# Kernel tuning notes

Measured on AMD Instinct MI355X. Metric: run time of the kernel, lower is better.

Reference implementation:

```python
import jax, jax.numpy as jnp
import numpy as np

FEAT_STRIDE = 8
BASE_SCALES = jnp.array([16.0, 9.0, 14.0, 21.0, 33.0, 54.0, 93.0], dtype=jnp.float32)
SCALE = 1.0
N_PRE_NMS = 6000
N_POST_NMS = 300
NMS_THRESH = 0.7
MIN_SIZE = 16.0


def setup_inputs() -> dict:
    key = jax.random.key(0)
    ks = jax.random.split(key, 8)
    C, M, H, W = 512, 512, 128, 128
    return {
        "x": jax.random.normal(ks[0], (1, C, H, W), jnp.float32),
        "skeleton_mask": jax.random.randint(ks[1], (H, W), 0, 2).astype(jnp.int32),
        "conv1_w": jax.random.normal(ks[2], (M, C, 3, 3), jnp.float32) * 0.01,
        "conv1_b": jnp.zeros((M,), jnp.float32),
        "loc_w": jax.random.normal(ks[3], (4, M), jnp.float32) * 0.01,
        "loc_b": jnp.zeros((4,), jnp.float32),
        "cls_w": jax.random.normal(ks[4], (7, M), jnp.float32) * 0.01,
        "cls_b": jnp.zeros((7,), jnp.float32),
        "cos_w": jax.random.normal(ks[5], (1, M), jnp.float32) * 0.01,
        "cos_b": jnp.zeros((1,), jnp.float32),
        "img_h": 1024,
        "img_w": 1024,
    }


def _loc2bbox(anchor, loc):
    # anchor, loc: (R,4) yxyx / (dy,dx,dh,dw)
    h = anchor[:, 2] - anchor[:, 0]
    w = anchor[:, 3] - anchor[:, 1]
    cy = anchor[:, 0] + 0.5 * h
    cx = anchor[:, 1] + 0.5 * w
    ncy = loc[:, 0] * h + cy
    ncx = loc[:, 1] * w + cx
    nh = jnp.exp(loc[:, 2]) * h
    nw = jnp.exp(loc[:, 3]) * w
    return jnp.stack([ncy - 0.5 * nh, ncx - 0.5 * nw, ncy + 0.5 * nh, ncx + 0.5 * nw], axis=1)


def _nms(boxes, scores, thresh, n_out):
    # greedy NMS with fixed number of output slots (jit-compatible)
    ys0, xs0, ys1, xs1 = boxes[:, 0], boxes[:, 1], boxes[:, 2], boxes[:, 3]
    areas = (ys1 - ys0) * (xs1 - xs0)

    def body(k, state):
        live, keep_idx, keep_valid = state
        s = jnp.where(live, scores, -jnp.inf)
        i = jnp.argmax(s)
        valid = s[i] > -jnp.inf
        yy0 = jnp.maximum(ys0, boxes[i, 0])
        xx0 = jnp.maximum(xs0, boxes[i, 1])
        yy1 = jnp.minimum(ys1, boxes[i, 2])
        xx1 = jnp.minimum(xs1, boxes[i, 3])
        inter = jnp.maximum(yy1 - yy0, 0.0) * jnp.maximum(xx1 - xx0, 0.0)
        iou = inter / (areas + areas[i] - inter + 1e-9)
        live = live & (iou <= thresh)  # removes i itself (iou==1)
        keep_idx = keep_idx.at[k].set(jnp.where(valid, i, 0).astype(jnp.int32))
        keep_valid = keep_valid.at[k].set(valid)
        return live, keep_idx, keep_valid

    live0 = jnp.ones(boxes.shape[0], dtype=bool)
    idx0 = jnp.zeros((n_out,), jnp.int32)
    val0 = jnp.zeros((n_out,), bool)
    _, keep_idx, keep_valid = jax.lax.fori_loop(0, n_out, body, (live0, idx0, val0))
    return keep_idx, keep_valid


def reference(x, skeleton_mask, conv1_w, conv1_b, loc_w, loc_b, cls_w, cls_b, cos_w, cos_b, img_h, img_w):
    n, C, hh, ww = x.shape
    # conv1 + relu + skeleton attention mask (broadcast over all channels as in repeat)
    h = jax.lax.conv_general_dilated(
        x, conv1_w, window_strides=(1, 1), padding="SAME",
        dimension_numbers=("NCHW", "OIHW", "NCHW")) + conv1_b[None, :, None, None]
    h = jax.nn.relu(h) * skeleton_mask.astype(h.dtype)[None, None, :, :]

    # 1x1 heads as einsum
    rpn_locs = (jnp.einsum("nchw,oc->nhwo", h, loc_w) + loc_b).reshape(n, -1, 4)
    rpn_cos = jax.nn.sigmoid(jnp.einsum("nchw,oc->nhwo", h, cos_w) + cos_b).reshape(n, -1, 1)
    rpn_cls = jnp.einsum("nchw,oc->nhwo", h, cls_w) + cls_b  # (n, hh, ww, 7)
    p = jax.nn.softmax(rpn_cls, axis=-1)
    rpn_fg_scores = (1.0 - p[..., 0]).reshape(n, -1)
    rpn_cls_flat = rpn_cls.reshape(-1, 7)
    p_flat = p.reshape(-1, 7)

    # anchor generation (data dependent)
    assignment = jnp.argmax(p_flat, axis=1)                    # (HW,)
    ascale = BASE_SCALES[assignment] * SCALE
    acos = rpn_cos[0, :, 0]
    acos = jnp.where(acos == 0, acos + 1e-5, acos)
    hvec = ascale * jnp.sqrt(1.0 / (acos * acos) - 1.0)
    anchor_h = jnp.full_like(ascale, hvec[0])  # faithful to original _cos2hw [0] broadcast
    anchor_w = ascale
    sy, sx = jnp.meshgrid(jnp.arange(hh, dtype=jnp.float32) * FEAT_STRIDE,
                          jnp.arange(ww, dtype=jnp.float32) * FEAT_STRIDE, indexing="ij")
    ay = sy.ravel() + FEAT_STRIDE / 2.0
    ax = sx.ravel() + FEAT_STRIDE / 2.0
    anchor = jnp.stack([ay - 0.5 * anchor_h, ax - 0.5 * anchor_w,
                        ay + 0.5 * anchor_h, ax + 0.5 * anchor_w], axis=1)

    # keepa: only anchors assigned to a foreground scale class (mask instead of gather)
    keep_mask = assignment > 0

    # ProposalCreator: decode, clip, min-size filter, top-k, NMS
    roi = _loc2bbox(anchor, rpn_locs[0])
    roi = jnp.stack([jnp.clip(roi[:, 0], 0.0, float(img_h)),
                     jnp.clip(roi[:, 1], 0.0, float(img_w)),
                     jnp.clip(roi[:, 2], 0.0, float(img_h)),
                     jnp.clip(roi[:, 3], 0.0, float(img_w))], axis=1)
    hs = roi[:, 2] - roi[:, 0]
    ws = roi[:, 3] - roi[:, 1]
    valid = keep_mask & (hs >= MIN_SIZE * SCALE) & (ws >= MIN_SIZE * SCALE)
    scores = jnp.where(valid, rpn_fg_scores[0], -jnp.inf)

    top_scores, order = jax.lax.top_k(scores, N_PRE_NMS)
    cand = roi[order]                                           # (N_PRE_NMS, 4)
    cand = jnp.where(jnp.isfinite(top_scores)[:, None], cand, 0.0)
    keep_idx, keep_valid = _nms(cand, top_scores, NMS_THRESH, N_POST_NMS)

    rois = jnp.where(keep_valid[:, None], cand[keep_idx], 0.0)   # (N_POST_NMS, 4) padded
    roi_scores = jnp.where(keep_valid, top_scores[keep_idx], 0.0)
    roi_indices = jnp.zeros((N_POST_NMS,), jnp.int32)
    old_rois = cand                                              # pre-NMS candidates

    return (rpn_locs, rois, roi_indices, anchor, rpn_cls_flat, rpn_cos, roi_scores, old_rois)
```

## Files before the change

kernel.cpp:

```cpp
#include <hip/hip_runtime.h>
#include <math.h>

#define HH 128
#define WW 128
#define CIN 512
#define NPIX 16384
#define NPRE 6000
#define NPOST 300
#define NMW 94

#define WS_XS1    0ull
#define WS_XS2    4194304ull
#define WS_XS3    8388608ull
#define WS_WB1    12582912ull
#define WS_WB2    13762560ull
#define WS_WB3    14942208ull
#define WS_LIST   16121856ull
#define WS_NACT   16138240ull
#define WS_MASK   16138248ull
#define WS_LOG    17266248ull
#define WS_ROI    17659464ull
#define WS_SC32   17725000ull
#define WS_CAND   17741384ull
#define WS_TOPS   17765384ull

#define O_LOCS   0
#define O_ROIS   65536
#define O_RIDX   66736
#define O_ANCHOR 67036
#define O_CLS    132572
#define O_COS    247260
#define O_RSC    263644
#define O_OLD    263944

typedef short bf16x8 __attribute__((ext_vector_type(8)));
typedef float f32x4 __attribute__((ext_vector_type(4)));

__device__ __forceinline__ float exp32(float x) { return (float)exp((double)x); }
__device__ __forceinline__ float sqrt32(float x) { return (float)sqrt((double)x); }

__device__ __forceinline__ unsigned short bf16t(float v) {
  return (unsigned short)(__float_as_uint(v) >> 16);
}
__device__ __forceinline__ float bf2f(unsigned short u) {
  return __uint_as_float((unsigned)u << 16);
}
__device__ __forceinline__ void split3(float v, unsigned short& s1,
                                       unsigned short& s2, unsigned short& s3) {
  s1 = bf16t(v);
  float r = v - bf2f(s1);
  s2 = bf16t(r);
  float r2 = r - bf2f(s2);
  s3 = bf16t(r2);
}

__global__ __launch_bounds__(256) void prep_kernel(
    const float* __restrict__ x, const float* __restrict__ w,
    unsigned short* __restrict__ xs1, unsigned short* __restrict__ xs2,
    unsigned short* __restrict__ xs3, unsigned short* __restrict__ wb1,
    unsigned short* __restrict__ wb2, unsigned short* __restrict__ wb3,
    double* __restrict__ logits, const int* __restrict__ mask,
    int* __restrict__ list, int* __restrict__ nact) {
  int b = blockIdx.x;
  int tid = threadIdx.x;
  if (b < 2048) {
    __shared__ float t[64][65];
    int p0 = (b & 255) * 64;
    int c0 = (b >> 8) * 64;
    int lo = tid & 63;
    int q = tid >> 6;
#pragma unroll
    for (int ii = 0; ii < 16; ++ii) {
      int cc = q + ii * 4;
      t[cc][lo] = x[(size_t)(c0 + cc) * NPIX + p0 + lo];
    }
    __syncthreads();
#pragma unroll
    for (int ii = 0; ii < 16; ++ii) {
      int pp = q + ii * 4;
      float v = t[lo][pp];
      unsigned short s1, s2, s3;
      split3(v, s1, s2, s3);
      size_t addr = (size_t)(p0 + pp) * 512 + c0 + lo;
      xs1[addr] = s1; xs2[addr] = s2; xs3[addr] = s3;
    }
  } else if (b < 2495) {
    int i = (b - 2048) * 256 + tid;
    const int stride = 447 * 256;
    for (; i < NPIX * 12; i += stride) logits[i] = 0.0;
  } else if (b == 2495) {
    __shared__ int sc[256];
    int base = tid << 6;
    int cnt = 0;
    for (int i = 0; i < 64; ++i) cnt += (mask[base + i] != 0);
    sc[tid] = cnt;
    __syncthreads();
    for (int off = 1; off < 256; off <<= 1) {
      int v = 0;
      if (tid >= off) v = sc[tid - off];
      __syncthreads();
      sc[tid] += v;
      __syncthreads();
    }
    int pos = sc[tid] - cnt;
    for (int i = 0; i < 64; ++i)
      if (mask[base + i] != 0) list[pos++] = base + i;
    if (tid == 255) nact[0] = sc[255];
  } else {
    int id = (b - 2496) * 256 + tid;
    const int stride = 2048 * 256;
    for (; id < 9 * 512 * 512; id += stride) {
      int ce = id & 7;
      int oc = (id >> 3) & 511;
      int rest = id >> 12;
      int j = rest >> 6;
      int cb = rest & 63;
      int c = cb * 8 + ce;
      float v = w[(size_t)oc * 4608 + c * 9 + j];
      unsigned short s1, s2, s3;
      split3(v, s1, s2, s3);
      wb1[id] = s1; wb2[id] = s2; wb3[id] = s3;
    }
  }
}

__global__ __launch_bounds__(256, 2) void conv_bf16_kernel(
    const unsigned short* __restrict__ xs1, const unsigned short* __restrict__ xs2,
    const unsigned short* __restrict__ xs3, const unsigned short* __restrict__ wb1,
    const unsigned short* __restrict__ wb2, const unsigned short* __restrict__ wb3,
    const float* __restrict__ bias, const float* __restrict__ loc_w,
    const float* __restrict__ cls_w, const float* __restrict__ cos_w,
    const int* __restrict__ list, const int* __restrict__ nact,
    double* __restrict__ logits) {
  int tid = threadIdx.x;
  int lane = tid & 63;
  int wv = tid >> 6;
  int n = nact[0];
  int ntg = (n + 63) >> 6;
  int total = ntg << 3;
  int lin = blockIdx.x;
  int xcd = lin & 7;
  int slot = lin >> 3;
  int wpx = (total + 7) >> 3;
  int w = xcd * wpx + slot;
  if (slot >= wpx || w >= total) return;
  int tg = w >> 3;
  int m0 = (w & 7) << 6;
  int tile = tg * 4 + wv;
  if (tile * 16 >= n) return;
  int col = lane & 15;
  int kk = lane >> 4;

  int slotp = tile * 16 + col;
  int p = (slotp < n) ? list[slotp] : -1;
  bool pv = (p >= 0);
  int py = p >> 7, px = p & 127;

  int offj[9];
  bool valj[9];
#pragma unroll
  for (int j = 0; j < 9; ++j) {
    int dy = j / 3 - 1, dx = j % 3 - 1;
    int yy = py + dy, xx = px + dx;
    bool v = pv && (yy >= 0) && (yy < HH) && (xx >= 0) && (xx < WW);
    valj[j] = v;
    offj[j] = v ? (yy * WW + xx) : 0;
  }

  f32x4 acc[4];
#pragma unroll
  for (int nf = 0; nf < 4; ++nf) acc[nf] = (f32x4){0.f, 0.f, 0.f, 0.f};

  const bf16x8 zzv = (bf16x8){0, 0, 0, 0, 0, 0, 0, 0};
  int ka = kk * 8;
  int bcol[4];
#pragma unroll
  for (int nf = 0; nf < 4; ++nf) bcol[nf] = (m0 + nf * 16 + col) * 8;

  for (int c0 = 0; c0 < CIN; c0 += 32) {
    int kc = c0 + ka;
    int cb = kc >> 3;
#pragma unroll
    for (int j = 0; j < 9; ++j) {
      size_t axi = (size_t)offj[j] * 512 + kc;
      bf16x8 a1 = *(const bf16x8*)(xs1 + axi);
      bf16x8 a2 = *(const bf16x8*)(xs2 + axi);
      bf16x8 a3 = *(const bf16x8*)(xs3 + axi);
      a1 = valj[j] ? a1 : zzv;
      a2 = valj[j] ? a2 : zzv;
      a3 = valj[j] ? a3 : zzv;
      int wjb = (j * 64 + cb) * 4096;
      bf16x8 B1[4], B2[4], B3[4];
#pragma unroll
      for (int nf = 0; nf < 4; ++nf) {
        B1[nf] = *(const bf16x8*)(wb1 + wjb + bcol[nf]);
        B2[nf] = *(const bf16x8*)(wb2 + wjb + bcol[nf]);
        B3[nf] = *(const bf16x8*)(wb3 + wjb + bcol[nf]);
      }
#pragma unroll
      for (int nf = 0; nf < 4; ++nf)
        acc[nf] = __builtin_amdgcn_mfma_f32_16x16x32_bf16(a1, B1[nf], acc[nf], 0, 0, 0);
#pragma unroll
      for (int nf = 0; nf < 4; ++nf)
        acc[nf] = __builtin_amdgcn_mfma_f32_16x16x32_bf16(a1, B2[nf], acc[nf], 0, 0, 0);
#pragma unroll
      for (int nf = 0; nf < 4; ++nf)
        acc[nf] = __builtin_amdgcn_mfma_f32_16x16x32_bf16(a2, B1[nf], acc[nf], 0, 0, 0);
#pragma unroll
      for (int nf = 0; nf < 4; ++nf)
        acc[nf] = __builtin_amdgcn_mfma_f32_16x16x32_bf16(a1, B3[nf], acc[nf], 0, 0, 0);
#pragma unroll
      for (int nf = 0; nf < 4; ++nf)
        acc[nf] = __builtin_amdgcn_mfma_f32_16x16x32_bf16(a2, B2[nf], acc[nf], 0, 0, 0);
#pragma unroll
      for (int nf = 0; nf < 4; ++nf)
        acc[nf] = __builtin_amdgcn_mfma_f32_16x16x32_bf16(a3, B1[nf], acc[nf], 0, 0, 0);
    }
  }

#pragma unroll
  for (int jj = 0; jj < 4; ++jj) {
    float hvj[4];
#pragma unroll
    for (int nf = 0; nf < 4; ++nf) {
      float bb = bias[m0 + nf * 16 + col];
      hvj[nf] = fmaxf(__fadd_rn(acc[nf][jj], bb), 0.f);
    }
    int s2 = tile * 16 + kk * 4 + jj;
    bool wr = (col == 0) && (s2 < n);
    int pix = wr ? list[s2] : 0;
#pragma unroll
    for (int r = 0; r < 12; ++r) {
      double t = 0.0;
#pragma unroll
      for (int nf = 0; nf < 4; ++nf) {
        int oc = m0 + nf * 16 + col;
        float wh = (r < 4) ? loc_w[r * 512 + oc]
                           : (r < 11) ? cls_w[(r - 4) * 512 + oc] : cos_w[oc];
        t += (double)hvj[nf] * (double)wh;
      }
#pragma unroll
      for (int o = 8; o; o >>= 1) t += __shfl_xor(t, o, 16);
      if (wr) atomicAdd(&logits[(size_t)pix * 12 + r], t);
    }
  }
}

__global__ __launch_bounds__(256) void finroi_kernel(
    const double* __restrict__ logits, const float* __restrict__ loc_b,
    const float* __restrict__ cls_b, const float* __restrict__ cos_b,
    const int* __restrict__ img_h, const int* __restrict__ img_w,
    float* __restrict__ out, float* __restrict__ roi,
    float* __restrict__ scores32) {
  int p = blockIdx.x * 256 + threadIdx.x;
  const double* lg = &logits[(size_t)p * 12];
  float l4[4];
#pragma unroll
  for (int o = 0; o < 4; ++o) {
    l4[o] = (float)(lg[o] + (double)loc_b[o]);
    out[O_LOCS + p * 4 + o] = l4[o];
  }
  double cl[7];
#pragma unroll
  for (int i = 0; i < 7; ++i) {
    cl[i] = lg[4 + i] + (double)cls_b[i];
    out[O_CLS + p * 7 + i] = (float)cl[i];
  }
  double z = lg[11] + (double)cos_b[0];
  double sig = 1.0 / (1.0 + exp(-z));
  out[O_COS + p] = (float)sig;
  double pm = cl[0];
  int ai = 0;
#pragma unroll
  for (int i = 1; i < 7; ++i)
    if (cl[i] > pm) { pm = cl[i]; ai = i; }
  double mx = cl[0];
#pragma unroll
  for (int i = 1; i < 7; ++i) mx = fmax(mx, cl[i]);
  double S = 0.0;
#pragma unroll
  for (int i = 0; i < 7; ++i) S += exp(cl[i] - mx);
  double p0 = exp(cl[0] - mx) / S;
  float fg = (float)(1.0 - p0);
  const float BS[7] = {16.f, 9.f, 14.f, 21.f, 33.f, 54.f, 93.f};
  float ascale_p = BS[ai];
  double cl0[7];
#pragma unroll
  for (int i = 0; i < 7; ++i) cl0[i] = logits[4 + i] + (double)cls_b[i];
  double pm0 = cl0[0];
  int ai0 = 0;
#pragma unroll
  for (int i = 1; i < 7; ++i)
    if (cl0[i] > pm0) { pm0 = cl0[i]; ai0 = i; }
  float ascale0 = BS[ai0];
  double z0 = logits[11] + (double)cos_b[0];
  float a0 = (float)(1.0 / (1.0 + exp(-z0)));
  if (a0 == 0.0f) a0 = __fadd_rn(a0, 1e-5f);
  float t1 = __fmul_rn(a0, a0);
  float t2 = __fdiv_rn(1.0f, t1);
  float t3 = __fsub_rn(t2, 1.0f);
  float anchor_h = __fmul_rn(ascale0, sqrt32(t3));
  float anchor_w = ascale_p;
  float ay = __fadd_rn((float)(p >> 7) * 8.0f, 4.0f);
  float ax = __fadd_rn((float)(p & 127) * 8.0f, 4.0f);
  float A0 = __fsub_rn(ay, __fmul_rn(0.5f, anchor_h));
  float A1 = __fsub_rn(ax, __fmul_rn(0.5f, anchor_w));
  float A2 = __fadd_rn(ay, __fmul_rn(0.5f, anchor_h));
  float A3 = __fadd_rn(ax, __fmul_rn(0.5f, anchor_w));
  *(float4*)&out[O_ANCHOR + p * 4] = make_float4(A0, A1, A2, A3);
  float hA = __fsub_rn(A2, A0), wA = __fsub_rn(A3, A1);
  float cy = __fadd_rn(A0, __fmul_rn(0.5f, hA));
  float cx = __fadd_rn(A1, __fmul_rn(0.5f, wA));
  float ncy = __fadd_rn(__fmul_rn(l4[0], hA), cy);
  float ncx = __fadd_rn(__fmul_rn(l4[1], wA), cx);
  float nh = __fmul_rn(exp32(l4[2]), hA);
  float nw = __fmul_rn(exp32(l4[3]), wA);
  float b0 = __fsub_rn(ncy, __fmul_rn(0.5f, nh));
  float b1 = __fsub_rn(ncx, __fmul_rn(0.5f, nw));
  float b2 = __fadd_rn(ncy, __fmul_rn(0.5f, nh));
  float b3 = __fadd_rn(ncx, __fmul_rn(0.5f, nw));
  float IH = (float)img_h[0], IW = (float)img_w[0];
  b0 = fminf(fmaxf(b0, 0.f), IH);
  b1 = fminf(fmaxf(b1, 0.f), IW);
  b2 = fminf(fmaxf(b2, 0.f), IH);
  b3 = fminf(fmaxf(b3, 0.f), IW);
  *(float4*)&roi[p * 4] = make_float4(b0, b1, b2, b3);
  float hs = __fsub_rn(b2, b0), wd = __fsub_rn(b3, b1);
  bool valid = (ai > 0) && (hs >= 16.f) && (wd >= 16.f);
  scores32[p] = valid ? fg : -INFINITY;
}

__global__ __launch_bounds__(256) void rank_kernel(
    const float* __restrict__ scores32, const float* __restrict__ roi,
    float* __restrict__ out, float* __restrict__ cand, float* __restrict__ tops) {
  __shared__ unsigned long long kt[2048];
  int tid = threadIdx.x;
  int i = blockIdx.x * 256 + tid;
  unsigned u = __float_as_uint(scores32[i]);
  u = (u & 0x80000000u) ? ~u : (u | 0x80000000u);
  unsigned long long mykey = ((unsigned long long)u << 32) | (unsigned)(16383 - i);
  int rank = 0;
  for (int t0 = 0; t0 < 16384; t0 += 2048) {
    __syncthreads();
#pragma unroll
    for (int s = 0; s < 8; ++s) {
      int j = t0 + s * 256 + tid;
      unsigned uj = __float_as_uint(scores32[j]);
      uj = (uj & 0x80000000u) ? ~uj : (uj | 0x80000000u);
      kt[s * 256 + tid] = ((unsigned long long)uj << 32) | (unsigned)(16383 - j);
    }
    __syncthreads();
    for (int t = 0; t < 2048; ++t)
      rank += (kt[t] > mykey) ? 1 : 0;
  }
  if (rank < NPRE) {
    float s = scores32[i];
    float4 b = make_float4(0.f, 0.f, 0.f, 0.f);
    if (isfinite(s)) b = *(const float4*)&roi[i * 4];
    ((float4*)(out + O_OLD))[rank] = b;
    ((float4*)cand)[rank] = b;
    tops[rank] = s;
  }
}

__global__ __launch_bounds__(64) void nms_mask_kernel(
    const float* __restrict__ cand, unsigned long long* __restrict__ mask) {
  __shared__ float cy0[64], cx0[64], cy1[64], cx1[64], car[64];
  int bw = blockIdx.x;
  int bj = blockIdx.y;
  int t = threadIdx.x;
  int c = bw * 64 + t;
  if (c < NPRE) {
    float4 b = ((const float4*)cand)[c];
    cy0[t] = b.x; cx0[t] = b.y; cy1[t] = b.z; cx1[t] = b.w;
    car[t] = __fmul_rn(__fsub_rn(b.z, b.x), __fsub_rn(b.w, b.y));
  } else {
    cy0[t] = 0.f; cx0[t] = 0.f; cy1[t] = 0.f; cx1[t] = 0.f; car[t] = 0.f;
  }
  __syncthreads();
  int r = bj * 64 + t;
  if (r >= NPRE) return;
  float4 rb = ((const float4*)cand)[r];
  float rar = __fmul_rn(__fsub_rn(rb.z, rb.x), __fsub_rn(rb.w, rb.y));
  unsigned long long bits = 0;
#pragma unroll 4
  for (int b = 0; b < 64; ++b) {
    int j = bw * 64 + b;
    float yy0 = fmaxf(cy0[b], rb.x), xx0 = fmaxf(cx0[b], rb.y);
    float yy1 = fminf(cy1[b], rb.z), xx1 = fminf(cx1[b], rb.w);
    float inter = __fmul_rn(fmaxf(__fsub_rn(yy1, yy0), 0.f),
                            fmaxf(__fsub_rn(xx1, xx0), 0.f));
    float den = __fadd_rn(__fsub_rn(__fadd_rn(car[b], rar), inter), 1e-9f);
    float iou = __fdiv_rn(inter, den);
    if (j > r && j < NPRE && iou > 0.7f)
      bits |= 1ull << b;
  }
  mask[(size_t)r * NMW + bw] = bits;
}

__global__ __launch_bounds__(128) void nms_reduce_kernel(
    const float* __restrict__ cand, const float* __restrict__ tops,
    const unsigned long long* __restrict__ mask, float* __restrict__ out) {
  __shared__ unsigned long long remv[NMW];
  __shared__ int red2[2];
  int tid = threadIdx.x;
  int lane = tid & 63, wid = tid >> 6;
  if (tid < NMW) remv[tid] = 0ull;
  __syncthreads();
  int kdone = NPOST;
  for (int k = 0; k < NPOST; ++k) {
    int cnd = 0x7FFFFFFF;
    if (tid < NMW) {
      unsigned long long avail = ~remv[tid];
      if (tid == NMW - 1) avail &= (1ull << (NPRE - (NMW - 1) * 64)) - 1;
      if (avail) cnd = (tid << 6) + (int)__builtin_ctzll(avail);
    }
#pragma unroll
    for (int off = 32; off; off >>= 1) {
      int o = __shfl_xor(cnd, off, 64);
      cnd = min(cnd, o);
    }
    if (lane == 0) red2[wid] = cnd;
    __syncthreads();
    int pick = min(red2[0], red2[1]);
    bool valid = (pick != 0x7FFFFFFF) && (tops[pick] != -INFINITY);
    if (!valid) { kdone = k; break; }
    if (tid == 0) {
      float4 b = ((const float4*)cand)[pick];
      out[O_ROIS + k * 4 + 0] = b.x;
      out[O_ROIS + k * 4 + 1] = b.y;
      out[O_ROIS + k * 4 + 2] = b.z;
      out[O_ROIS + k * 4 + 3] = b.w;
      out[O_RSC + k] = tops[pick];
    }
    if (tid < NMW) {
      unsigned long long m = mask[(size_t)pick * NMW + tid];
      if (tid == (pick >> 6)) m |= 1ull << (pick & 63);
      remv[tid] |= m;
    }
    __syncthreads();
  }
  for (int t = kdone + tid; t < NPOST; t += 128) {
    out[O_ROIS + t * 4 + 0] = 0.f;
    out[O_ROIS + t * 4 + 1] = 0.f;
    out[O_ROIS + t * 4 + 2] = 0.f;
    out[O_ROIS + t * 4 + 3] = 0.f;
    out[O_RSC + t] = 0.f;
  }
  for (int t = tid; t < NPOST; t += 128) out[O_RIDX + t] = 0.f;
}

extern "C" void kernel_launch(void* const* d_in, const int* in_sizes, int n_in,
                              void* d_out, int out_size, void* d_ws, size_t ws_size,
                              hipStream_t stream) {
  (void)in_sizes; (void)n_in; (void)out_size; (void)ws_size;
  const float* x      = (const float*)d_in[0];
  const int*   skel   = (const int*)d_in[1];
  const float* conv_w = (const float*)d_in[2];
  const float* conv_b = (const float*)d_in[3];
  const float* loc_w  = (const float*)d_in[4];
  const float* loc_b  = (const float*)d_in[5];
  const float* cls_w  = (const float*)d_in[6];
  const float* cls_b  = (const float*)d_in[7];
  const float* cos_w  = (const float*)d_in[8];
  const float* cos_b  = (const float*)d_in[9];
  const int*   img_h  = (const int*)d_in[10];
  const int*   img_w  = (const int*)d_in[11];
  float* out = (float*)d_out;
  float* ws  = (float*)d_ws;

  unsigned short* xs1 = (unsigned short*)(ws + WS_XS1);
  unsigned short* xs2 = (unsigned short*)(ws + WS_XS2);
  unsigned short* xs3 = (unsigned short*)(ws + WS_XS3);
  unsigned short* wb1 = (unsigned short*)(ws + WS_WB1);
  unsigned short* wb2 = (unsigned short*)(ws + WS_WB2);
  unsigned short* wb3 = (unsigned short*)(ws + WS_WB3);
  int*    list     = (int*)(ws + WS_LIST);
  int*    nact     = (int*)(ws + WS_NACT);
  unsigned long long* nmsmask = (unsigned long long*)(ws + WS_MASK);
  double* logits   = (double*)(ws + WS_LOG);
  float*  roi      = ws + WS_ROI;
  float*  scores32 = ws + WS_SC32;
  float*  cand     = ws + WS_CAND;
  float*  tops     = ws + WS_TOPS;

  hipLaunchKernelGGL(prep_kernel, dim3(4544), dim3(256), 0, stream, x, conv_w,
                     xs1, xs2, xs3, wb1, wb2, wb3, logits, skel, list, nact);
  hipLaunchKernelGGL(conv_bf16_kernel, dim3(2048), dim3(256), 0, stream, xs1, xs2,
                     xs3, wb1, wb2, wb3, conv_b, loc_w, cls_w, cos_w, list, nact,
                     logits);
  hipLaunchKernelGGL(finroi_kernel, dim3(64), dim3(256), 0, stream, logits, loc_b,
                     cls_b, cos_b, img_h, img_w, out, roi, scores32);
  hipLaunchKernelGGL(rank_kernel, dim3(64), dim3(256), 0, stream, scores32, roi, out,
                     cand, tops);
  hipLaunchKernelGGL(nms_mask_kernel, dim3(NMW, NMW), dim3(64), 0, stream, cand,
                     nmsmask);
  hipLaunchKernelGGL(nms_reduce_kernel, dim3(1), dim3(128), 0, stream, cand, tops,
                     nmsmask, out);
}
```

Baseline: 1.070 ms.

## Process two 16-pixel tiles per wave to reuse weight fragments

Each wave now computes two 16-pixel subtiles against the same 64 output channels, so each loaded B fragment (three bf16 splits) feeds twice as many MFMAs and per-MFMA weight traffic is halved. Out-of-bounds neighbours now point at a zeroed padding row in the split-input buffers instead of using per-load selects, and the workspace offsets shift to make room for that row. The grid is halved to match. The cost is doubled accumulator and A-fragment registers, which may pressure occupancy under launch_bounds(256,2).

```diff
diff --git a/kernel.cpp b/kernel.cpp
--- a/kernel.cpp
+++ b/kernel.cpp
@@ -8,21 +8,22 @@
 #define NPRE 6000
 #define NPOST 300
 #define NMW 94
+#define ZROW 16384
 
 #define WS_XS1    0ull
-#define WS_XS2    4194304ull
-#define WS_XS3    8388608ull
-#define WS_WB1    12582912ull
-#define WS_WB2    13762560ull
-#define WS_WB3    14942208ull
-#define WS_LIST   16121856ull
-#define WS_NACT   16138240ull
-#define WS_MASK   16138248ull
-#define WS_LOG    17266248ull
-#define WS_ROI    17659464ull
-#define WS_SC32   17725000ull
-#define WS_CAND   17741384ull
-#define WS_TOPS   17765384ull
+#define WS_XS2    4194560ull
+#define WS_XS3    8389120ull
+#define WS_WB1    12583680ull
+#define WS_WB2    13763328ull
+#define WS_WB3    14942976ull
+#define WS_LIST   16122624ull
+#define WS_NACT   16139008ull
+#define WS_MASK   16139012ull
+#define WS_LOG    17267012ull
+#define WS_ROI    17660228ull
+#define WS_SC32   17725764ull
+#define WS_CAND   17742148ull
+#define WS_TOPS   17766148ull
 
 #define O_LOCS   0
 #define O_ROIS   65536
@@ -85,6 +86,12 @@
       xs1[addr] = s1; xs2[addr] = s2; xs3[addr] = s3;
     }
   } else if (b < 2495) {
+    if (b == 2048) {
+      for (int i = tid; i < 512; i += 256) {
+        size_t z = (size_t)ZROW * 512 + i;
+        xs1[z] = 0; xs2[z] = 0; xs3[z] = 0;
+      }
+    }
     int i = (b - 2048) * 256 + tid;
     const int stride = 447 * 256;
     for (; i < NPIX * 12; i += stride) logits[i] = 0.0;
@@ -136,7 +143,7 @@
   int lane = tid & 63;
   int wv = tid >> 6;
   int n = nact[0];
-  int ntg = (n + 63) >> 6;
+  int ntg = (n + 127) >> 7;
   int total = ntg << 3;
   int lin = blockIdx.x;
   int xcd = lin & 7;
@@ -146,33 +153,33 @@
   if (slot >= wpx || w >= total) return;
   int tg = w >> 3;
   int m0 = (w & 7) << 6;
-  int tile = tg * 4 + wv;
-  if (tile * 16 >= n) return;
+  int base = tg * 128 + wv * 32;
+  if (base >= n) return;
   int col = lane & 15;
   int kk = lane >> 4;
-
-  int slotp = tile * 16 + col;
-  int p = (slotp < n) ? list[slotp] : -1;
-  bool pv = (p >= 0);
-  int py = p >> 7, px = p & 127;
-
-  int offj[9];
-  bool valj[9];
-#pragma unroll
-  for (int j = 0; j < 9; ++j) {
-    int dy = j / 3 - 1, dx = j % 3 - 1;
-    int yy = py + dy, xx = px + dx;
-    bool v = pv && (yy >= 0) && (yy < HH) && (xx >= 0) && (xx < WW);
-    valj[j] = v;
-    offj[j] = v ? (yy * WW + xx) : 0;
-  }
-
-  f32x4 acc[4];
-#pragma unroll
-  for (int nf = 0; nf < 4; ++nf) acc[nf] = (f32x4){0.f, 0.f, 0.f, 0.f};
-
-  const bf16x8 zzv = (bf16x8){0, 0, 0, 0, 0, 0, 0, 0};
   int ka = kk * 8;
+
+  int offj[2][9];
+#pragma unroll
+  for (int s = 0; s < 2; ++s) {
+    int slotp = base + s * 16 + col;
+    int p = (slotp < n) ? list[slotp] : -1;
+    int py = p >> 7, px = p & 127;
+#pragma unroll
+    for (int j = 0; j < 9; ++j) {
+      int dy = j / 3 - 1, dx = j % 3 - 1;
+      int yy = py + dy, xx = px + dx;
+      bool v = (p >= 0) && (yy >= 0) && (yy < HH) && (xx >= 0) && (xx < WW);
+      offj[s][j] = v ? (yy * WW + xx) : ZROW;
+    }
+  }
+
+  f32x4 acc[2][4];
+#pragma unroll
+  for (int s = 0; s < 2; ++s)
+#pragma unroll
+    for (int nf = 0; nf < 4; ++nf) acc[s][nf] = (f32x4){0.f, 0.f, 0.f, 0.f};
+
   int bcol[4];
 #pragma unroll
   for (int nf = 0; nf < 4; ++nf) bcol[nf] = (m0 + nf * 16 + col) * 8;
@@ -182,66 +189,60 @@
     int cb = kc >> 3;
 #pragma unroll
     for (int j = 0; j < 9; ++j) {
-      size_t axi = (size_t)offj[j] * 512 + kc;
-      bf16x8 a1 = *(const bf16x8*)(xs1 + axi);
-      bf16x8 a2 = *(const bf16x8*)(xs2 + axi);
-      bf16x8 a3 = *(const bf16x8*)(xs3 + axi);
-      a1 = valj[j] ? a1 : zzv;
-      a2 = valj[j] ? a2 : zzv;
-      a3 = valj[j] ? a3 : zzv;
+      bf16x8 a1[2], a2[2], a3[2];
+#pragma unroll
+      for (int s = 0; s < 2; ++s) {
+        size_t axi = (size_t)offj[s][j] * 512 + kc;
+        a1[s] = *(const bf16x8*)(xs1 + axi);
+        a2[s] = *(const bf16x8*)(xs2 + axi);
+        a3[s] = *(const bf16x8*)(xs3 + axi);
+      }
       int wjb = (j * 64 + cb) * 4096;
-      bf16x8 B1[4], B2[4], B3[4];
 #pragma unroll
       for (int nf = 0; nf < 4; ++nf) {
-        B1[nf] = *(const bf16x8*)(wb1 + wjb + bcol[nf]);
-        B2[nf] = *(const bf16x8*)(wb2 + wjb + bcol[nf]);
-        B3[nf] = *(const bf16x8*)(wb3 + wjb + bcol[nf]);
+        bf16x8 B1 = *(const bf16x8*)(wb1 + wjb + bcol[nf]);
+        bf16x8 B2 = *(const bf16x8*)(wb2 + wjb + bcol[nf]);
+        bf16x8 B3 = *(const bf16x8*)(wb3 + wjb + bcol[nf]);
+#pragma unroll
+        for (int s = 0; s < 2; ++s) {
+          acc[s][nf] = __builtin_amdgcn_mfma_f32_16x16x32_bf16(a1[s], B1, acc[s][nf], 0, 0, 0);
+          acc[s][nf] = __builtin_amdgcn_mfma_f32_16x16x32_bf16(a1[s], B2, acc[s][nf], 0, 0, 0);
+          acc[s][nf] = __builtin_amdgcn_mfma_f32_16x16x32_bf16(a2[s], B1, acc[s][nf], 0, 0, 0);
+          acc[s][nf] = __builtin_amdgcn_mfma_f32_16x16x32_bf16(a1[s], B3, acc[s][nf], 0, 0, 0);
+          acc[s][nf] = __builtin_amdgcn_mfma_f32_16x16x32_bf16(a2[s], B2, acc[s][nf], 0, 0, 0);
+          acc[s][nf] = __builtin_amdgcn_mfma_f32_16x16x32_bf16(a3[s], B1, acc[s][nf], 0, 0, 0);
+        }
       }
-#pragma unroll
-      for (int nf = 0; nf < 4; ++nf)
-        acc[nf] = __builtin_amdgcn_mfma_f32_16x16x32_bf16(a1, B1[nf], acc[nf], 0, 0, 0);
-#pragma unroll
-      for (int nf = 0; nf < 4; ++nf)
-        acc[nf] = __builtin_amdgcn_mfma_f32_16x16x32_bf16(a1, B2[nf], acc[nf], 0, 0, 0);
-#pragma unroll
-      for (int nf = 0; nf < 4; ++nf)
-        acc[nf] = __builtin_amdgcn_mfma_f32_16x16x32_bf16(a2, B1[nf], acc[nf], 0, 0, 0);
-#pragma unroll
-      for (int nf = 0; nf < 4; ++nf)
-        acc[nf] = __builtin_amdgcn_mfma_f32_16x16x32_bf16(a1, B3[nf], acc[nf], 0, 0, 0);
-#pragma unroll
-      for (int nf = 0; nf < 4; ++nf)
-        acc[nf] = __builtin_amdgcn_mfma_f32_16x16x32_bf16(a2, B2[nf], acc[nf], 0, 0, 0);
-#pragma unroll
-      for (int nf = 0; nf < 4; ++nf)
-        acc[nf] = __builtin_amdgcn_mfma_f32_16x16x32_bf16(a3, B1[nf], acc[nf], 0, 0, 0);
-    }
-  }
-
-#pragma unroll
-  for (int jj = 0; jj < 4; ++jj) {
-    float hvj[4];
-#pragma unroll
-    for (int nf = 0; nf < 4; ++nf) {
-      float bb = bias[m0 + nf * 16 + col];
-      hvj[nf] = fmaxf(__fadd_rn(acc[nf][jj], bb), 0.f);
-    }
-    int s2 = tile * 16 + kk * 4 + jj;
-    bool wr = (col == 0) && (s2 < n);
-    int pix = wr ? list[s2] : 0;
-#pragma unroll
-    for (int r = 0; r < 12; ++r) {
-      double t = 0.0;
+    }
+  }
+
+#pragma unroll
+  for (int s = 0; s < 2; ++s) {
+#pragma unroll
+    for (int jj = 0; jj < 4; ++jj) {
+      float hvj[4];
 #pragma unroll
       for (int nf = 0; nf < 4; ++nf) {
-        int oc = m0 + nf * 16 + col;
-        float wh = (r < 4) ? loc_w[r * 512 + oc]
-                           : (r < 11) ? cls_w[(r - 4) * 512 + oc] : cos_w[oc];
-        t += (double)hvj[nf] * (double)wh;
+        float bb = bias[m0 + nf * 16 + col];
+        hvj[nf] = fmaxf(__fadd_rn(acc[s][nf][jj], bb), 0.f);
       }
-#pragma unroll
-      for (int o = 8; o; o >>= 1) t += __shfl_xor(t, o, 16);
-      if (wr) atomicAdd(&logits[(size_t)pix * 12 + r], t);
+      int s2 = base + s * 16 + kk * 4 + jj;
+      bool wr = (col == 0) && (s2 < n);
+      int pix = wr ? list[s2] : 0;
+#pragma unroll
+      for (int r = 0; r < 12; ++r) {
+        double t = 0.0;
+#pragma unroll
+        for (int nf = 0; nf < 4; ++nf) {
+          int oc = m0 + nf * 16 + col;
+          float wh = (r < 4) ? loc_w[r * 512 + oc]
+                             : (r < 11) ? cls_w[(r - 4) * 512 + oc] : cos_w[oc];
+          t += (double)hvj[nf] * (double)wh;
+        }
+#pragma unroll
+        for (int o = 8; o; o >>= 1) t += __shfl_xor(t, o, 16);
+        if (wr) atomicAdd(&logits[(size_t)pix * 12 + r], t);
+      }
     }
   }
 }
@@ -486,7 +487,7 @@
 
   hipLaunchKernelGGL(prep_kernel, dim3(4544), dim3(256), 0, stream, x, conv_w,
                      xs1, xs2, xs3, wb1, wb2, wb3, logits, skel, list, nact);
-  hipLaunchKernelGGL(conv_bf16_kernel, dim3(2048), dim3(256), 0, stream, xs1, xs2,
+  hipLaunchKernelGGL(conv_bf16_kernel, dim3(1024), dim3(256), 0, stream, xs1, xs2,
                      xs3, wb1, wb2, wb3, conv_b, loc_w, cls_w, cos_w, list, nact,
                      logits);
   hipLaunchKernelGGL(finroi_kernel, dim3(64), dim3(256), 0, stream, logits, loc_b,
```

Result: slower. 1.108 ms (+3.5%).
